# Optimization experiments

Measured on AMD Instinct MI355X. Metric: run time of the kernel, lower is better.

## Reference

```python
import jax, jax.numpy as jnp
from jax import lax
import numpy as np

EPS = 1e-5
COMMITMENT = 0.25


def conv1d(x, w, b, pad):
    # x: [N,C,T], w: [O,I,K]
    y = lax.conv_general_dilated(x, w, window_strides=(1,), padding=[(pad, pad)],
                                 dimension_numbers=('NCH', 'OIH', 'NCH'))
    return y + b[None, :, None]


def batchnorm(x, g, b):
    # training-mode BN (PyTorch default): batch stats over (N, T), biased var
    m = jnp.mean(x, axis=(0, 2), keepdims=True)
    v = jnp.var(x, axis=(0, 2), keepdims=True)
    return (x - m) * lax.rsqrt(v + EPS) * g[None, :, None] + b[None, :, None]


def setup_inputs() -> dict:
    key = jax.random.key(0)
    ks = jax.random.split(key, 16)
    B, C_in, T = 16, 80, 4096
    H1, H2, D, K = 128, 256, 64, 512
    s = 0.05
    inp = {
        'x': jax.random.normal(ks[0], (B, C_in, T), jnp.float32),
        # encoder
        'enc_w1': jax.random.normal(ks[1], (H1, C_in, 3), jnp.float32) * s,
        'enc_b1': jnp.zeros((H1,), jnp.float32),
        'bn1_g': jnp.ones((H1,), jnp.float32), 'bn1_b': jnp.zeros((H1,), jnp.float32),
        'enc_w2': jax.random.normal(ks[2], (H2, H1, 3), jnp.float32) * s,
        'enc_b2': jnp.zeros((H2,), jnp.float32),
        'bn2_g': jnp.ones((H2,), jnp.float32), 'bn2_b': jnp.zeros((H2,), jnp.float32),
        'enc_w3': jax.random.normal(ks[3], (D, H2, 1), jnp.float32) * s,
        'enc_b3': jnp.zeros((D,), jnp.float32),
        # codebook, init uniform(-1/K, 1/K) like the torch module
        'codebook': jax.random.uniform(ks[4], (K, D), jnp.float32, -1.0 / K, 1.0 / K),
        # decoder (hidden_dims reversed: [256, 128])
        'dec_w1': jax.random.normal(ks[5], (H2, D, 3), jnp.float32) * s,
        'dec_b1': jnp.zeros((H2,), jnp.float32),
        'dbn1_g': jnp.ones((H2,), jnp.float32), 'dbn1_b': jnp.zeros((H2,), jnp.float32),
        'dec_w2': jax.random.normal(ks[6], (H1, H2, 3), jnp.float32) * s,
        'dec_b2': jnp.zeros((H1,), jnp.float32),
        'dbn2_g': jnp.ones((H1,), jnp.float32), 'dbn2_b': jnp.zeros((H1,), jnp.float32),
        'dec_w3': jax.random.normal(ks[7], (C_in, H1, 3), jnp.float32) * s,
        'dec_b3': jnp.zeros((C_in,), jnp.float32),
    }
    return inp


def _vqvae(x, enc_w1, enc_b1, bn1_g, bn1_b, enc_w2, enc_b2, bn2_g, bn2_b,
           enc_w3, enc_b3, codebook, dec_w1, dec_b1, dbn1_g, dbn1_b,
           dec_w2, dec_b2, dbn2_g, dbn2_b, dec_w3, dec_b3):
    # ---- Encoder ----
    h = jax.nn.relu(batchnorm(conv1d(x, enc_w1, enc_b1, 1), bn1_g, bn1_b))
    h = jax.nn.relu(batchnorm(conv1d(h, enc_w2, enc_b2, 1), bn2_g, bn2_b))
    z = conv1d(h, enc_w3, enc_b3, 0)  # [B, D, T]

    # ---- Vector Quantizer ----
    B, D, T = z.shape
    zt = jnp.transpose(z, (0, 2, 1))            # [B, T, D]
    flat = zt.reshape(-1, D)                    # [B*T, D]
    # squared L2 distances to codebook [B*T, K]
    d2 = (jnp.sum(flat * flat, axis=1, keepdims=True)
          + jnp.sum(codebook * codebook, axis=1)
          - 2.0 * flat @ codebook.T)
    idx = jnp.argmin(d2, axis=1)                # [B*T]
    quantized = codebook[idx].reshape(B, T, D)  # gather == onehot @ codebook

    e_latent_loss = jnp.mean((lax.stop_gradient(quantized) - zt) ** 2)
    q_latent_loss = jnp.mean((quantized - lax.stop_gradient(zt)) ** 2)
    vq_loss = q_latent_loss + COMMITMENT * e_latent_loss

    # straight-through estimator
    q_st = zt + lax.stop_gradient(quantized - zt)
    q_st = jnp.transpose(q_st, (0, 2, 1))       # [B, D, T]
    encoding_indices = idx.reshape(B, T)

    # ---- Decoder ----
    h = conv1d(q_st, dec_w1, dec_b1, 1)
    h = conv1d(jax.nn.relu(batchnorm(h, dbn1_g, dbn1_b)), dec_w2, dec_b2, 1)
    recon = conv1d(jax.nn.relu(batchnorm(h, dbn2_g, dbn2_b)), dec_w3, dec_b3, 1)
    return recon, vq_loss, encoding_indices


def reference(x, enc_w1, enc_b1, bn1_g, bn1_b, enc_w2, enc_b2, bn2_g, bn2_b,
              enc_w3, enc_b3, codebook, dec_w1, dec_b1, dbn1_g, dbn1_b,
              dec_w2, dec_b2, dbn2_g, dbn2_b, dec_w3, dec_b3):
    return _vqvae(x, enc_w1, enc_b1, bn1_g, bn1_b, enc_w2, enc_b2, bn2_g, bn2_b,
                  enc_w3, enc_b3, codebook, dec_w1, dec_b1, dbn1_g, dbn1_b,
                  dec_w2, dec_b2, dbn2_g, dbn2_b, dec_w3, dec_b3)
```

## Files before the change

### kernel.cpp

```cpp
#include <hip/hip_runtime.h>
#include <math.h>

#define N_B 16
#define T_LEN 4096

typedef float f32x4  __attribute__((ext_vector_type(4)));
typedef _Float16 half8 __attribute__((ext_vector_type(8)));

static const size_t OFF_A    = 0;
static const size_t OFF_B    = 8388608;
static const size_t OFF_Z    = 25165824;
static const size_t OFF_WS   = 29360128;
static const size_t OFF_CBS  = 29540352;
static const size_t OFF_C2   = 29683712;
static const size_t OFF_ST   = 29684736;
static const size_t OFF_LOSS = 29685760;

static const size_t WS_E1 = 0;
static const size_t WS_E2 = 36864;
static const size_t WS_E3 = 135168;
static const size_t WS_D1 = 0;
static const size_t WS_D2 = 49152;
static const size_t WS_D3 = 147456;

__device__ inline void f2h2(float v, short& hi, short& lo) {
    _Float16 h = (_Float16)v;
    float r = (v - (float)h) * 4096.0f;
    _Float16 l = (_Float16)r;
    hi = __builtin_bit_cast(short, h);
    lo = __builtin_bit_cast(short, l);
}
__device__ inline float h2f(short s) {
    return (float)__builtin_bit_cast(_Float16, s);
}

template<int C_IN, int C_OUT, int KS>
__device__ inline void wsplit_fill(const float* __restrict__ w,
                                   short* __restrict__ dst, int e) {
    int i  = e & 31;
    int r  = e >> 5;
    int co = r % C_OUT;
    int r2 = r / C_OUT;
    int k  = r2 % KS;
    int c  = r2 / KS;
    int ci = c * 32 + i;
    float v = (ci < C_IN) ? w[((size_t)co * C_IN + ci) * KS + k] : 0.f;
    short h, l; f2h2(v, h, l);
    size_t base = ((size_t)(c * KS + k) * 2 * C_OUT + co) * 32 + i;
    dst[base] = h;
    dst[base + (size_t)C_OUT * 32] = l;
}

__global__ __launch_bounds__(256) void prep_k(
        const float* __restrict__ w1, const float* __restrict__ w2,
        const float* __restrict__ w3, const float* __restrict__ cb,
        float* wsf) {
    int e = blockIdx.x * 256 + threadIdx.x;
    if (e < 36864)        wsplit_fill<80, 128, 3>(w1, (short*)(wsf + OFF_WS + WS_E1), e);
    else if (e < 135168)  wsplit_fill<128, 256, 3>(w2, (short*)(wsf + OFF_WS + WS_E2), e - 36864);
    else if (e < 151552)  wsplit_fill<256, 64, 1>(w3, (short*)(wsf + OFF_WS + WS_E3), e - 135168);
    else if (e < 152064) {
        int c = e - 151552;
        const float* p = cb + (size_t)c * 64;
        double s = 0.0;
        for (int d = 0; d < 64; ++d) { double v = p[d]; s += v * v; }
        wsf[OFF_C2 + c] = (float)s;
    } else if (e < 184832) {
        int e2   = e - 152064;
        int i    = e2 & 31;
        int r    = e2 >> 5;
        int code = r & 511;
        int ks   = r >> 9;
        float v  = cb[(size_t)code * 64 + ks * 32 + i];
        short h, l; f2h2(v, h, l);
        short* dst = (short*)(wsf + OFF_CBS);
        dst[((size_t)(ks * 2 + 0) * 512 + code) * 32 + i] = h;
        dst[((size_t)(ks * 2 + 1) * 512 + code) * 32 + i] = l;
    } else if (e == 184832) {
        *(double*)(wsf + OFF_LOSS) = 0.0;
    }
}

__global__ __launch_bounds__(256) void prep2_k(
        const float* __restrict__ wd1, const float* __restrict__ wd2,
        const float* __restrict__ wd3, float* wsf) {
    int e = blockIdx.x * 256 + threadIdx.x;
    if (e < 49152)        wsplit_fill<64, 256, 3>(wd1, (short*)(wsf + OFF_WS + WS_D1), e);
    else if (e < 147456)  wsplit_fill<256, 128, 3>(wd2, (short*)(wsf + OFF_WS + WS_D2), e - 49152);
    else if (e < 178176)  wsplit_fill<128, 80, 3>(wd3, (short*)(wsf + OFF_WS + WS_D3), e - 147456);
}

template<int C_IN, int C_OUT, int KS, bool BN_IN, bool STATS>
__global__ __launch_bounds__(512, 4) void fconv_k(
        const float* __restrict__ x, const short* __restrict__ wsp,
        const float* __restrict__ bias, const float2* __restrict__ stats,
        float* __restrict__ out, float2* __restrict__ part) {
    constexpr int NCH  = (C_IN + 31) / 32;
    constexpr int HALO = KS / 2;
    constexpr int TT   = 128;
    constexpr int WT   = (KS == 1) ? 2 : 1;
    constexpr int WCO  = 8 / WT;
    constexpr int HT   = TT / WT;
    constexpr int NTT  = HT / 16;
    constexpr int NTILE = T_LEN / TT;
    constexpr int XR   = TT + KS - 1;
    constexpr int RS   = 72;
    constexpr int LO   = 40;
    constexpr int TQ   = TT / 4;

    __shared__ __align__(16) short xs[2][XR * RS];

    const int tid  = threadIdx.x;
    const int lane = tid & 63;
    const int wv   = tid >> 6;
    const int wvc  = wv % WCO;
    const int wvt  = wv / WCO;
    const int ln   = lane & 15;
    const int q    = lane >> 4;

    const int n    = blockIdx.x / NTILE;
    const int t0   = (blockIdx.x % NTILE) * TT;
    const int co0  = blockIdx.y * (WCO * 16);
    const int co_l = co0 + wvc * 16 + ln;

    auto stage = [&](int c, short* buf) {
        for (int e = tid; e < 32 * TQ; e += 512) {
            const int ci  = e / TQ;
            const int tq  = e % TQ;
            const int cig = c * 32 + ci;
            float v[4] = {0.f, 0.f, 0.f, 0.f};
            if (cig < C_IN) {
                const float* xp = x + ((size_t)(n * C_IN + cig)) * T_LEN + t0 + tq;
#pragma unroll
                for (int j = 0; j < 4; ++j) v[j] = xp[TQ * j];
                if (BN_IN) {
                    float2 s = stats[cig];
#pragma unroll
                    for (int j = 0; j < 4; ++j) v[j] = fmaxf(fmaf(v[j], s.x, s.y), 0.f);
                }
            }
#pragma unroll
            for (int j = 0; j < 4; ++j) {
                short h, l; f2h2(v[j], h, l);
                short* p = &buf[(HALO + tq + TQ * j) * RS + ci];
                p[0]  = h;
                p[LO] = l;
            }
        }
        if (KS == 3) {
            if (tid < 64) {
                const int ci   = tid & 31;
                const int side = tid >> 5;
                const int cig  = c * 32 + ci;
                const int gt   = side ? (t0 + TT) : (t0 - 1);
                float v = 0.f;
                if (cig < C_IN && gt >= 0 && gt < T_LEN) {
                    v = x[((size_t)(n * C_IN + cig)) * T_LEN + gt];
                    if (BN_IN) {
                        float2 s = stats[cig];
                        v = fmaxf(fmaf(v, s.x, s.y), 0.f);
                    }
                }
                short h, l; f2h2(v, h, l);
                short* p = &buf[(side ? (XR - 1) : 0) * RS + ci];
                p[0] = h; p[LO] = l;
            }
        }
    };

    f32x4 a0[NTT], a1[NTT];
#pragma unroll
    for (int tt = 0; tt < NTT; ++tt)
#pragma unroll
        for (int i = 0; i < 4; ++i) { a0[tt][i] = 0.f; a1[tt][i] = 0.f; }

    stage(0, xs[0]);

#pragma unroll 1
    for (int c = 0; c < NCH; ++c) {
        half8 ah[KS], al[KS];
        {
            half8 z = {0, 0, 0, 0, 0, 0, 0, 0};
#pragma unroll
            for (int k = 0; k < KS; ++k) {
                const short* wp = wsp
                    + ((size_t)(c * KS + k) * 2 * C_OUT + co_l) * 32 + q * 8;
                ah[k] = (co_l < C_OUT) ? *(const half8*)wp : z;
                al[k] = (co_l < C_OUT) ? *(const half8*)(wp + (size_t)C_OUT * 32) : z;
            }
        }

        __syncthreads();
        if (c + 1 < NCH) stage(c + 1, xs[(c + 1) & 1]);

        const short* sb = xs[c & 1];
#pragma unroll
        for (int k = 0; k < KS; ++k) {
#pragma unroll
            for (int tt = 0; tt < NTT; ++tt) {
                const short* xr = &sb[(wvt * HT + tt * 16 + ln + k) * RS + q * 8];
                half8 bh = *(const half8*)&xr[0];
                half8 bl = *(const half8*)&xr[LO];
                a0[tt] = __builtin_amdgcn_mfma_f32_16x16x32_f16(ah[k], bh, a0[tt], 0, 0, 0);
                a1[tt] = __builtin_amdgcn_mfma_f32_16x16x32_f16(ah[k], bl, a1[tt], 0, 0, 0);
                a1[tt] = __builtin_amdgcn_mfma_f32_16x16x32_f16(al[k], bh, a1[tt], 0, 0, 0);
            }
        }
    }

    const int plinear = blockIdx.y * (N_B * NTILE) + blockIdx.x;
#pragma unroll
    for (int r = 0; r < 4; ++r) {
        const int co = co0 + wvc * 16 + q * 4 + r;
        float s1 = 0.f, s2 = 0.f;
        if (co < C_OUT) {
            const float bv = bias[co];
            float* op = out + ((size_t)(n * C_OUT + co)) * T_LEN + t0 + wvt * HT + ln;
#pragma unroll
            for (int tt = 0; tt < NTT; ++tt) {
                const float v = fmaf(a1[tt][r], 0.000244140625f, a0[tt][r]) + bv;
                op[tt * 16] = v;
                if (STATS) { s1 += v; s2 = fmaf(v, v, s2); }
            }
        }
        if (STATS) {
#pragma unroll
            for (int off = 1; off <= 8; off <<= 1) {
                s1 += __shfl_xor(s1, off);
                s2 += __shfl_xor(s2, off);
            }
            if (ln == 0)
                part[(size_t)plinear * 128 + wvc * 16 + q * 4 + r] =
                    make_float2(s1, s2);
        }
    }
}

__global__ __launch_bounds__(256) void stats_k(
        const float2* __restrict__ part, const float* __restrict__ g,
        const float* __restrict__ b, float2* __restrict__ stats) {
    const int c = blockIdx.x;
    const int tid = threadIdx.x;
    double s1 = 0.0, s2 = 0.0;
    for (int j = tid; j < 512; j += 256) {
        float2 v = part[((size_t)(c >> 7) * 512 + j) * 128 + (c & 127)];
        s1 += (double)v.x; s2 += (double)v.y;
    }
    __shared__ double r1[256], r2[256];
    r1[tid] = s1; r2[tid] = s2;
    __syncthreads();
    for (int s = 128; s > 0; s >>= 1) {
        if (tid < s) { r1[tid] += r1[tid + s]; r2[tid] += r2[tid + s]; }
        __syncthreads();
    }
    if (tid == 0) {
        double m   = r1[0] / 65536.0;
        double var = r2[0] / 65536.0 - m * m;
        double sc  = (double)g[c] / sqrt(var + 1e-5);
        stats[c] = make_float2((float)sc, (float)((double)b[c] - m * sc));
    }
}

__global__ __launch_bounds__(256) void vq_k(
        const float* __restrict__ z, const float* __restrict__ cb,
        const short* __restrict__ cbs, const float* __restrict__ c2,
        float* __restrict__ q, float* __restrict__ idx_out,
        double* __restrict__ loss) {
    __shared__ __align__(16) float zs[64 * 68];
    __shared__ __align__(16) short zh[64 * 136];
    __shared__ float  c2s[512];
    __shared__ float  szf_s[64];
    __shared__ int    idxs[64];
    __shared__ double dred[256];

    const int tid  = threadIdx.x;
    const int lane = tid & 63;
    const int wv   = tid >> 6;
    const int ln   = lane & 15;
    const int q4   = lane >> 4;
    const int n    = blockIdx.x >> 6;
    const int t0   = (blockIdx.x & 63) * 64;

    for (int e = tid; e < 512; e += 256) c2s[e] = c2[e];
    for (int e = tid; e < 1024; e += 256) {
        const int d  = e >> 4;
        const int tq = e & 15;
        const float* zp = z + ((size_t)(n * 64 + d)) * T_LEN + t0 + tq;
        const int ks = d >> 5, i = d & 31;
#pragma unroll
        for (int j = 0; j < 4; ++j) {
            const int t = tq + 16 * j;
            float v = zp[16 * j];
            zs[t * 68 + d] = v;
            short h, l; f2h2(v, h, l);
            zh[t * 136 + (ks * 2 + 0) * 32 + i] = h;
            zh[t * 136 + (ks * 2 + 1) * 32 + i] = l;
        }
    }
    __syncthreads();
    if (tid < 64) {
        double s = 0.0;
        const float* zr = &zs[tid * 68];
        for (int d = 0; d < 64; ++d) { double v = zr[d]; s += v * v; }
        szf_s[tid] = (float)s;
    }
    __syncthreads();

    const short* zr = &zh[(wv * 16 + ln) * 136 + q4 * 8];
    const half8 bh0 = *(const half8*)&zr[0];
    const half8 bl0 = *(const half8*)&zr[32];
    const half8 bh1 = *(const half8*)&zr[64];
    const half8 bl1 = *(const half8*)&zr[96];
    const float As  = szf_s[wv * 16 + ln];

    float bs = 3.0e38f;
    int   bi = 1 << 30;

#pragma unroll 4
    for (int ct = 0; ct < 32; ++ct) {
        const short* ap = cbs + ((size_t)(ct * 16 + ln)) * 32 + q4 * 8;
        const half8 ah0 = *(const half8*)&ap[0];
        const half8 al0 = *(const half8*)&ap[512 * 32];
        const half8 ah1 = *(const half8*)&ap[2 * 512 * 32];
        const half8 al1 = *(const half8*)&ap[3 * 512 * 32];
        f32x4 a0 = {0.f, 0.f, 0.f, 0.f};
        f32x4 a1 = {0.f, 0.f, 0.f, 0.f};
        a0 = __builtin_amdgcn_mfma_f32_16x16x32_f16(ah0, bh0, a0, 0, 0, 0);
        a1 = __builtin_amdgcn_mfma_f32_16x16x32_f16(ah0, bl0, a1, 0, 0, 0);
        a1 = __builtin_amdgcn_mfma_f32_16x16x32_f16(al0, bh0, a1, 0, 0, 0);
        a0 = __builtin_amdgcn_mfma_f32_16x16x32_f16(ah1, bh1, a0, 0, 0, 0);
        a1 = __builtin_amdgcn_mfma_f32_16x16x32_f16(ah1, bl1, a1, 0, 0, 0);
        a1 = __builtin_amdgcn_mfma_f32_16x16x32_f16(al1, bh1, a1, 0, 0, 0);
#pragma unroll
        for (int r = 0; r < 4; ++r) {
            const int code = ct * 16 + q4 * 4 + r;
            const float m32 = fmaf(a1[r], 0.000244140625f, a0[r]);
            const float A   = As + c2s[code];
            const float s   = A - 2.0f * m32;
            if (s < bs || (s == bs && code < bi)) { bs = s; bi = code; }
        }
    }
#pragma unroll
    for (int off = 16; off <= 32; off <<= 1) {
        const float os = __shfl_xor(bs, off);
        const int   oi = __shfl_xor(bi, off);
        if (os < bs || (os == bs && oi < bi)) { bs = os; bi = oi; }
    }
    if (q4 == 0) {
        const int t = wv * 16 + ln;
        idxs[t] = bi;
        idx_out[(size_t)n * T_LEN + t0 + t] = (float)bi;
    }
    __syncthreads();

    {
        const int g = tid >> 6, t = tid & 63;
        const int bi2 = idxs[t];
        double ls = 0.0;
        for (int dd = 0; dd < 16; ++dd) {
            const int d = g * 16 + dd;
            const float qv = cb[(size_t)bi2 * 64 + d];
            const float zv = zs[t * 68 + d];
            const double df = (double)qv - (double)zv;
            ls += df * df;
            q[((size_t)(n * 64 + d)) * T_LEN + t0 + t] = qv;
        }
        dred[tid] = ls;
    }
    __syncthreads();
    for (int s = 128; s > 0; s >>= 1) {
        if (tid < s) dred[tid] += dred[tid + s];
        __syncthreads();
    }
    if (tid == 0) atomicAdd(loss, dred[0]);
}

__global__ void fin_k(const double* __restrict__ loss, float* __restrict__ out) {
    if (threadIdx.x == 0 && blockIdx.x == 0)
        out[0] = (float)(1.25 * (*loss) / 4194304.0);
}

extern "C" void kernel_launch(void* const* d_in, const int* in_sizes, int n_in,
                              void* d_out, int out_size, void* d_ws, size_t ws_size,
                              hipStream_t stream) {
    const float* x      = (const float*)d_in[0];
    const float* enc_w1 = (const float*)d_in[1];
    const float* enc_b1 = (const float*)d_in[2];
    const float* bn1_g  = (const float*)d_in[3];
    const float* bn1_b  = (const float*)d_in[4];
    const float* enc_w2 = (const float*)d_in[5];
    const float* enc_b2 = (const float*)d_in[6];
    const float* bn2_g  = (const float*)d_in[7];
    const float* bn2_b  = (const float*)d_in[8];
    const float* enc_w3 = (const float*)d_in[9];
    const float* enc_b3 = (const float*)d_in[10];
    const float* cb     = (const float*)d_in[11];
    const float* dec_w1 = (const float*)d_in[12];
    const float* dec_b1 = (const float*)d_in[13];
    const float* dbn1_g = (const float*)d_in[14];
    const float* dbn1_b = (const float*)d_in[15];
    const float* dec_w2 = (const float*)d_in[16];
    const float* dec_b2 = (const float*)d_in[17];
    const float* dbn2_g = (const float*)d_in[18];
    const float* dbn2_b = (const float*)d_in[19];
    const float* dec_w3 = (const float*)d_in[20];
    const float* dec_b3 = (const float*)d_in[21];

    float* wsf   = (float*)d_ws;
    float* outf  = (float*)d_out;
    float* A     = wsf + OFF_A;
    float* Bb    = wsf + OFF_B;
    float* Z     = wsf + OFF_Z;
    float2* st   = (float2*)(wsf + OFF_ST);
    double* lossp = (double*)(wsf + OFF_LOSS);

    const short* wsE1 = (const short*)(wsf + OFF_WS + WS_E1);
    const short* wsE2 = (const short*)(wsf + OFF_WS + WS_E2);
    const short* wsE3 = (const short*)(wsf + OFF_WS + WS_E3);
    const short* wsD1 = (const short*)(wsf + OFF_WS + WS_D1);
    const short* wsD2 = (const short*)(wsf + OFF_WS + WS_D2);
    const short* wsD3 = (const short*)(wsf + OFF_WS + WS_D3);
    const short* cbs  = (const short*)(wsf + OFF_CBS);

    float2* pE1 = (float2*)Bb;
    float2* pE2 = (float2*)Z;
    float2* pD1 = (float2*)A;
    float2* pD2 = (float2*)(wsf + OFF_B + 4194304);

    prep_k<<<723, 256, 0, stream>>>(enc_w1, enc_w2, enc_w3, cb, wsf);

    fconv_k<80, 128, 3, false, true><<<dim3(512, 1), 512, 0, stream>>>(
        x, wsE1, enc_b1, nullptr, A, pE1);
    stats_k<<<128, 256, 0, stream>>>(pE1, bn1_g, bn1_b, st);
    fconv_k<128, 256, 3, true, true><<<dim3(512, 2), 512, 0, stream>>>(
        A, wsE2, enc_b2, st, Bb, pE2);
    stats_k<<<256, 256, 0, stream>>>(pE2, bn2_g, bn2_b, st);
    fconv_k<256, 64, 1, true, false><<<dim3(512, 1), 512, 0, stream>>>(
        Bb, wsE3, enc_b3, st, Z, nullptr);

    prep2_k<<<696, 256, 0, stream>>>(dec_w1, dec_w2, dec_w3, wsf);

    vq_k<<<1024, 256, 0, stream>>>(Z, cb, cbs, wsf + OFF_C2, Z,
                                   outf + 5242881, lossp);
    fin_k<<<1, 64, 0, stream>>>(lossp, outf + 5242880);

    fconv_k<64, 256, 3, false, true><<<dim3(512, 2), 512, 0, stream>>>(
        Z, wsD1, dec_b1, nullptr, Bb, pD1);
    stats_k<<<256, 256, 0, stream>>>(pD1, dbn1_g, dbn1_b, st);
    fconv_k<256, 128, 3, true, true><<<dim3(512, 1), 512, 0, stream>>>(
        Bb, wsD2, dec_b2, st, A, pD2);
    stats_k<<<128, 256, 0, stream>>>(pD2, dbn2_g, dbn2_b, st);
    fconv_k<128, 80, 3, true, false><<<dim3(512, 1), 512, 0, stream>>>(
        A, wsD3, dec_b3, st, outf, nullptr);
}
```

Before: 364.2 us.

## Give each wave two output-channel subtiles to reuse staged input fragments

The conv kernel's wave layout changes so each wave computes two 16-row output-channel subtiles over a smaller time span, reusing each loaded B fragment from LDS across both subtiles. Weight fragments are now loaded per kernel tap inside the loop instead of all at once, and the per-block channel tile depends on C_OUT. Partial BN statistics are now written per wave time-slice, which doubles the partial count that stats_k reduces. The aim is fewer LDS reads per MFMA, at the cost of more accumulator registers and possibly lower occupancy.

```diff
diff --git a/kernel.cpp b/kernel.cpp
--- a/kernel.cpp
+++ b/kernel.cpp
@@ -98,8 +98,9 @@
     constexpr int NCH  = (C_IN + 31) / 32;
     constexpr int HALO = KS / 2;
     constexpr int TT   = 128;
-    constexpr int WT   = (KS == 1) ? 2 : 1;
-    constexpr int WCO  = 8 / WT;
+    constexpr int CO_TILE = (C_OUT >= 128) ? 128 : 64;
+    constexpr int WP   = CO_TILE / 32;
+    constexpr int WT   = 8 / WP;
     constexpr int HT   = TT / WT;
     constexpr int NTT  = HT / 16;
     constexpr int NTILE = T_LEN / TT;
@@ -113,15 +114,14 @@
     const int tid  = threadIdx.x;
     const int lane = tid & 63;
     const int wv   = tid >> 6;
-    const int wvc  = wv % WCO;
-    const int wvt  = wv / WCO;
+    const int wvp  = wv % WP;
+    const int wvt  = wv / WP;
     const int ln   = lane & 15;
     const int q    = lane >> 4;
 
     const int n    = blockIdx.x / NTILE;
     const int t0   = (blockIdx.x % NTILE) * TT;
-    const int co0  = blockIdx.y * (WCO * 16);
-    const int co_l = co0 + wvc * 16 + ln;
+    const int co0  = blockIdx.y * CO_TILE;
 
     auto stage = [&](int c, short* buf) {
         for (int e = tid; e < 32 * TQ; e += 512) {
@@ -168,70 +168,78 @@
         }
     };
 
-    f32x4 a0[NTT], a1[NTT];
-#pragma unroll
-    for (int tt = 0; tt < NTT; ++tt)
-#pragma unroll
-        for (int i = 0; i < 4; ++i) { a0[tt][i] = 0.f; a1[tt][i] = 0.f; }
+    f32x4 a0[2][NTT], a1[2][NTT];
+#pragma unroll
+    for (int cs = 0; cs < 2; ++cs)
+#pragma unroll
+        for (int tt = 0; tt < NTT; ++tt)
+#pragma unroll
+            for (int i = 0; i < 4; ++i) { a0[cs][tt][i] = 0.f; a1[cs][tt][i] = 0.f; }
 
     stage(0, xs[0]);
 
 #pragma unroll 1
     for (int c = 0; c < NCH; ++c) {
-        half8 ah[KS], al[KS];
-        {
-            half8 z = {0, 0, 0, 0, 0, 0, 0, 0};
-#pragma unroll
-            for (int k = 0; k < KS; ++k) {
-                const short* wp = wsp
-                    + ((size_t)(c * KS + k) * 2 * C_OUT + co_l) * 32 + q * 8;
-                ah[k] = (co_l < C_OUT) ? *(const half8*)wp : z;
-                al[k] = (co_l < C_OUT) ? *(const half8*)(wp + (size_t)C_OUT * 32) : z;
-            }
-        }
-
         __syncthreads();
         if (c + 1 < NCH) stage(c + 1, xs[(c + 1) & 1]);
 
         const short* sb = xs[c & 1];
 #pragma unroll
         for (int k = 0; k < KS; ++k) {
+            half8 ah[2], al[2];
+            {
+                half8 z = {0, 0, 0, 0, 0, 0, 0, 0};
+#pragma unroll
+                for (int cs = 0; cs < 2; ++cs) {
+                    const int co_l = co0 + (wvp * 2 + cs) * 16 + ln;
+                    const short* wp = wsp
+                        + ((size_t)(c * KS + k) * 2 * C_OUT + co_l) * 32 + q * 8;
+                    ah[cs] = (co_l < C_OUT) ? *(const half8*)wp : z;
+                    al[cs] = (co_l < C_OUT) ? *(const half8*)(wp + (size_t)C_OUT * 32) : z;
+                }
+            }
 #pragma unroll
             for (int tt = 0; tt < NTT; ++tt) {
                 const short* xr = &sb[(wvt * HT + tt * 16 + ln + k) * RS + q * 8];
                 half8 bh = *(const half8*)&xr[0];
                 half8 bl = *(const half8*)&xr[LO];
-                a0[tt] = __builtin_amdgcn_mfma_f32_16x16x32_f16(ah[k], bh, a0[tt], 0, 0, 0);
-                a1[tt] = __builtin_amdgcn_mfma_f32_16x16x32_f16(ah[k], bl, a1[tt], 0, 0, 0);
-                a1[tt] = __builtin_amdgcn_mfma_f32_16x16x32_f16(al[k], bh, a1[tt], 0, 0, 0);
-            }
-        }
-    }
-
-    const int plinear = blockIdx.y * (N_B * NTILE) + blockIdx.x;
-#pragma unroll
-    for (int r = 0; r < 4; ++r) {
-        const int co = co0 + wvc * 16 + q * 4 + r;
-        float s1 = 0.f, s2 = 0.f;
-        if (co < C_OUT) {
-            const float bv = bias[co];
-            float* op = out + ((size_t)(n * C_OUT + co)) * T_LEN + t0 + wvt * HT + ln;
-#pragma unroll
-            for (int tt = 0; tt < NTT; ++tt) {
-                const float v = fmaf(a1[tt][r], 0.000244140625f, a0[tt][r]) + bv;
-                op[tt * 16] = v;
-                if (STATS) { s1 += v; s2 = fmaf(v, v, s2); }
-            }
-        }
-        if (STATS) {
-#pragma unroll
-            for (int off = 1; off <= 8; off <<= 1) {
-                s1 += __shfl_xor(s1, off);
-                s2 += __shfl_xor(s2, off);
-            }
-            if (ln == 0)
-                part[(size_t)plinear * 128 + wvc * 16 + q * 4 + r] =
-                    make_float2(s1, s2);
+#pragma unroll
+                for (int cs = 0; cs < 2; ++cs) {
+                    a0[cs][tt] = __builtin_amdgcn_mfma_f32_16x16x32_f16(ah[cs], bh, a0[cs][tt], 0, 0, 0);
+                    a1[cs][tt] = __builtin_amdgcn_mfma_f32_16x16x32_f16(ah[cs], bl, a1[cs][tt], 0, 0, 0);
+                    a1[cs][tt] = __builtin_amdgcn_mfma_f32_16x16x32_f16(al[cs], bh, a1[cs][tt], 0, 0, 0);
+                }
+            }
+        }
+    }
+
+    const int plinear = (blockIdx.y * gridDim.x + blockIdx.x) * WT + wvt;
+#pragma unroll
+    for (int cs = 0; cs < 2; ++cs) {
+#pragma unroll
+        for (int r = 0; r < 4; ++r) {
+            const int co = co0 + (wvp * 2 + cs) * 16 + q * 4 + r;
+            float s1 = 0.f, s2 = 0.f;
+            if (co < C_OUT) {
+                const float bv = bias[co];
+                float* op = out + ((size_t)(n * C_OUT + co)) * T_LEN + t0 + wvt * HT + ln;
+#pragma unroll
+                for (int tt = 0; tt < NTT; ++tt) {
+                    const float v = fmaf(a1[cs][tt][r], 0.000244140625f, a0[cs][tt][r]) + bv;
+                    op[tt * 16] = v;
+                    if (STATS) { s1 += v; s2 = fmaf(v, v, s2); }
+                }
+            }
+            if (STATS) {
+#pragma unroll
+                for (int off = 1; off <= 8; off <<= 1) {
+                    s1 += __shfl_xor(s1, off);
+                    s2 += __shfl_xor(s2, off);
+                }
+                if (ln == 0)
+                    part[(size_t)plinear * CO_TILE + (wvp * 2 + cs) * 16 + q * 4 + r] =
+                        make_float2(s1, s2);
+            }
         }
     }
 }
@@ -242,8 +250,8 @@
     const int c = blockIdx.x;
     const int tid = threadIdx.x;
     double s1 = 0.0, s2 = 0.0;
-    for (int j = tid; j < 512; j += 256) {
-        float2 v = part[((size_t)(c >> 7) * 512 + j) * 128 + (c & 127)];
+    for (int j = tid; j < 1024; j += 256) {
+        float2 v = part[((size_t)(c >> 7) * 1024 + j) * 128 + (c & 127)];
         s1 += (double)v.x; s2 += (double)v.y;
     }
     __shared__ double r1[256], r2[256];
```

New measurement: 387.5 us. +6.4%, slower.
